# Optimization experiments

Measured on AMD Instinct MI355X. Metric: run time of the kernel, lower is better.

The kernel has to match this reference:

```python
import jax, jax.numpy as jnp
import numpy as np

TOP_K = 2
EPS = 1e-9


def setup_inputs() -> dict:
    key = jax.random.key(0)
    ks = jax.random.split(key, 5)
    B, S, D, H, E, G = 4, 2048, 1024, 1024, 8, 256
    x = jax.random.normal(ks[0], (B, S, D), dtype=jnp.float32)
    # gate MLP (top_k_gating with hidden_size=gating_size)
    Wg1 = jax.random.normal(ks[1], (D, G), dtype=jnp.float32) * (1.0 / np.sqrt(D))
    Wg2 = jax.random.normal(ks[2], (G, E), dtype=jnp.float32) * (1.0 / np.sqrt(G))
    # experts: uniform(-1/D, 1/D) as in init_experts
    W_in = jax.random.uniform(ks[3], (E, D, H), dtype=jnp.float32, minval=-1.0 / D, maxval=1.0 / D)
    W_out = jax.random.uniform(ks[4], (E, H, D), dtype=jnp.float32, minval=-1.0 / D, maxval=1.0 / D)
    return {"x": x, "Wg1": Wg1, "Wg2": Wg2, "W_in": W_in, "W_out": W_out}


def _gate(xf, Wg1, Wg2):
    # gate MLP -> softmax probs over experts
    h = jnp.tanh(xf @ Wg1)                      # [N, G]
    probs = jax.nn.softmax(h @ Wg2, axis=-1)    # [N, E]
    top_v, top_i = jax.lax.top_k(probs, TOP_K)  # [N, k]
    N, E = probs.shape
    # dense gate matrix: zeros except top-k entries (== compute_gating combine weights)
    gates = jnp.zeros((N, E), probs.dtype).at[jnp.arange(N)[:, None], top_i].set(top_v)
    return gates, probs


def _mi_loss(probs):
    # mutual-information aux loss: minimize -(H(mean_p) - mean H(p))
    p_mean = probs.mean(axis=0)
    h_mean = -jnp.sum(p_mean * jnp.log(p_mean + EPS))
    mean_h = -jnp.mean(jnp.sum(probs * jnp.log(probs + EPS), axis=-1))
    return -h_mean + mean_h


def reference(x, Wg1, Wg2, W_in, W_out):
    B, S, D = x.shape
    xf = x.reshape(-1, D)                        # [N, D]
    gates, probs = _gate(xf, Wg1, Wg2)           # [N, E]
    # per-expert FFN: relu(x @ W_in[e]) @ W_out[e], combined with top-k gates.
    h = jnp.einsum('nd,edh->enh', xf, W_in)      # [E, N, H]
    h = jax.nn.relu(h)
    y = jnp.einsum('enh,ehd->end', h, W_out)     # [E, N, D]
    out = jnp.einsum('ne,end->nd', gates, y)     # gate-weighted combine
    loss = _mi_loss(probs)
    return out.reshape(B, S, D), loss
```

## Files before the change

### kernel.cpp

```cpp
#include <hip/hip_runtime.h>


#define N_TOK 8192
#define DIM   1024
#define HID   1024
#define NEXP  8
#define GDIM  256
#define NPAIR (N_TOK * 2)
#define HB_ROWS (NPAIR + 256)
#define MT2   72
#define GAP_P 2e-3f
#define SPLIT_SCALE 2048.0f

typedef __attribute__((ext_vector_type(4))) float    f32x4;
typedef __attribute__((ext_vector_type(8))) _Float16 f16x8;

static __device__ __forceinline__ void async_ld16(const void* g, void* l) {
  __builtin_amdgcn_global_load_lds(
      (const __attribute__((address_space(1))) unsigned int*)g,
      (__attribute__((address_space(3))) unsigned int*)l, 16, 0, 0);
}

__global__ __launch_bounds__(256) void prep1_kernel(const float* __restrict__ Wg1,
                                                    _Float16* __restrict__ WhT,
                                                    _Float16* __restrict__ WlT,
                                                    int* __restrict__ hdr) {
  __shared__ float t[64][65];
  int bx = blockIdx.x;
  int tid = threadIdx.x;
  if (bx < 64) {
    int k0 = (bx & 15) * 64, g0 = (bx >> 4) * 64;
    int col4 = tid & 15, ib = tid >> 4;
#pragma unroll
    for (int q = 0; q < 4; ++q) {
      int i = ib * 4 + q;
      *(float4*)&t[i][col4 * 4] = *(const float4*)&Wg1[(size_t)(k0 + i) * GDIM + g0 + col4 * 4];
    }
    __syncthreads();
#pragma unroll
    for (int q = 0; q < 2; ++q) {
      int c = tid * 2 + q;
      int j = c >> 3, i8 = (c & 7) * 8;
      f16x8 h, l;
#pragma unroll
      for (int k = 0; k < 8; ++k) {
        float v = t[i8 + k][j];
        _Float16 hi = (_Float16)v;
        h[k] = hi;
        l[k] = (_Float16)((v - (float)hi) * SPLIT_SCALE);
      }
      *(f16x8*)&WhT[(size_t)(g0 + j) * DIM + k0 + i8] = h;
      *(f16x8*)&WlT[(size_t)(g0 + j) * DIM + k0 + i8] = l;
    }
  } else {
    hdr[tid * 2 + 0] = 0;
    hdr[tid * 2 + 1] = 0;
  }
}

__global__ __launch_bounds__(256) void gate_cast_kernel(const float* __restrict__ x,
                                                        _Float16* __restrict__ xh,
                                                        const _Float16* __restrict__ WhT,
                                                        const _Float16* __restrict__ WlT,
                                                        const float* __restrict__ Wg2,
                                                        int* __restrict__ top_i,
                                                        float* __restrict__ top_v,
                                                        float* __restrict__ lossacc,
                                                        int* __restrict__ counts,
                                                        int* __restrict__ nflag,
                                                        int* __restrict__ flaglist,
                                                        const float* __restrict__ Win,
                                                        const float* __restrict__ Wout,
                                                        _Float16* __restrict__ WinT,
                                                        _Float16* __restrict__ WoutT) {
  __shared__ __align__(16) char smem[34816];
  int bx = blockIdx.x;
  int tid = threadIdx.x;

  if (bx >= 256) {
    float (*t)[65] = (float(*)[65])smem;
    int b = bx - 256;
    int z = b >> 8, rem = b & 255;
    const float* src = (z < NEXP ? Win : Wout) + (size_t)(z & 7) * DIM * HID;
    _Float16*    dst = (z < NEXP ? WinT : WoutT) + (size_t)(z & 7) * DIM * HID;
    int i0 = (rem & 15) * 64, j0 = (rem >> 4) * 64;
    int col4 = tid & 15, ib = tid >> 4;
#pragma unroll
    for (int q = 0; q < 4; ++q) {
      int i = ib * 4 + q;
      *(float4*)&t[i][col4 * 4] = *(const float4*)&src[(size_t)(i0 + i) * 1024 + j0 + col4 * 4];
    }
    __syncthreads();
#pragma unroll
    for (int q = 0; q < 2; ++q) {
      int c = tid * 2 + q;
      int j = c >> 3, i8 = (c & 7) * 8;
      f16x8 h;
#pragma unroll
      for (int k = 0; k < 8; ++k) h[k] = (_Float16)t[i8 + k][j];
      *(f16x8*)&dst[(size_t)(j0 + j) * 1024 + i0 + i8] = h;
    }
    return;
  }

  _Float16* Ah = (_Float16*)smem;
  _Float16* Bh = (_Float16*)(smem + 2048);
  _Float16* Bl = (_Float16*)(smem + 18432);
  __shared__ float psum[8];
  __shared__ float entsum;
  __shared__ int cnts[8];
  int m0 = bx * 32;
  int lane = tid & 63, wave = tid >> 6;
  int wr = (wave >> 1) * 16;
  int wc = (wave & 1) * 128;
  if (tid < 8) { psum[tid] = 0.f; cnts[tid] = 0; }
  if (tid == 0) entsum = 0.f;

  int arow = tid >> 2, aslt = tid & 3;
  size_t axoff = (size_t)(m0 + arow) * DIM + ((aslt ^ ((arow >> 2) & 3)) << 3);
  _Float16* adst = Ah + tid * 8;
  int srcslot = ((lane & 3) ^ ((lane >> 4) & 3)) << 3;
  size_t bsrc[4];
#pragma unroll
  for (int p = 0; p < 4; ++p)
    bsrc[p] = (size_t)(wave * 16 + p * 64 + (lane >> 2)) * DIM + srcslot;
  int rdoff = ((lane >> 4) ^ ((lane >> 2) & 3)) << 3;
  f32x4 acc[8] = {}, accl[8] = {};

  for (int k0 = 0; k0 < DIM; k0 += 32) {
    __syncthreads();
    if (tid < 128) {
      float4 v0 = *(const float4*)(x + axoff + k0);
      float4 v1 = *(const float4*)(x + axoff + k0 + 4);
      f16x8 hv;
      hv[0] = (_Float16)v0.x; hv[1] = (_Float16)v0.y;
      hv[2] = (_Float16)v0.z; hv[3] = (_Float16)v0.w;
      hv[4] = (_Float16)v1.x; hv[5] = (_Float16)v1.y;
      hv[6] = (_Float16)v1.z; hv[7] = (_Float16)v1.w;
      *(f16x8*)adst = hv;
      *(f16x8*)(xh + axoff + k0) = hv;
    }
#pragma unroll
    for (int p = 0; p < 4; ++p) {
      async_ld16(WhT + bsrc[p] + k0, Bh + wave * 512 + p * 2048);
      async_ld16(WlT + bsrc[p] + k0, Bl + wave * 512 + p * 2048);
    }
    __syncthreads();
    f16x8 a = *(const f16x8*)&Ah[(wr + (lane & 15)) * 32 + rdoff];
#pragma unroll
    for (int n = 0; n < 8; ++n) {
      f16x8 bh = *(const f16x8*)&Bh[(wc + n * 16 + (lane & 15)) * 32 + rdoff];
      f16x8 bl = *(const f16x8*)&Bl[(wc + n * 16 + (lane & 15)) * 32 + rdoff];
      acc[n]  = __builtin_amdgcn_mfma_f32_16x16x32_f16(a, bh, acc[n], 0, 0, 0);
      accl[n] = __builtin_amdgcn_mfma_f32_16x16x32_f16(a, bl, accl[n], 0, 0, 0);
    }
  }
  __syncthreads();
  float (*hsm)[260] = (float(*)[260])smem;
#pragma unroll
  for (int n = 0; n < 8; ++n) {
#pragma unroll
    for (int i = 0; i < 4; ++i) {
      int row = wr + ((lane >> 4) << 2) + i;
      int col = wc + n * 16 + (lane & 15);
      hsm[row][col] = tanhf(acc[n][i] + accl[n][i] * (1.0f / SPLIT_SCALE));
    }
  }
  __syncthreads();

  int tok = tid >> 3, sl = tid & 7;
  float lg[8] = {0, 0, 0, 0, 0, 0, 0, 0};
#pragma unroll
  for (int j = 0; j < 32; ++j) {
    int g = sl + j * 8;
    float hv = hsm[tok][g];
#pragma unroll
    for (int e = 0; e < 8; ++e) lg[e] = fmaf(hv, Wg2[g * 8 + e], lg[e]);
  }
#pragma unroll
  for (int e = 0; e < 8; ++e) {
    lg[e] += __shfl_xor(lg[e], 4);
    lg[e] += __shfl_xor(lg[e], 2);
    lg[e] += __shfl_xor(lg[e], 1);
  }
  if (sl == 0) {
    int token = m0 + tok;
    float mx = lg[0];
#pragma unroll
    for (int e = 1; e < 8; ++e) mx = fmaxf(mx, lg[e]);
    float p[8], s = 0.f;
#pragma unroll
    for (int e = 0; e < 8; ++e) { p[e] = expf(lg[e] - mx); s += p[e]; }
    float inv = 1.f / s, ent = 0.f;
    int i0 = 0, i1 = 0;
    float v0 = -1.f, v1 = -1.f, v2 = -1.f;
#pragma unroll
    for (int e = 0; e < 8; ++e) {
      p[e] *= inv;
      ent += p[e] * logf(p[e] + 1e-9f);
      if (p[e] > v0)      { v2 = v1; v1 = v0; i1 = i0; v0 = p[e]; i0 = e; }
      else if (p[e] > v1) { v2 = v1; v1 = p[e]; i1 = e; }
      else if (p[e] > v2) { v2 = p[e]; }
    }
    top_i[token * 2 + 0] = i0; top_i[token * 2 + 1] = i1;
    top_v[token * 2 + 0] = v0; top_v[token * 2 + 1] = v1;
    if (v1 - v2 < GAP_P) {
      int ix = atomicAdd(nflag, 1);
      if (ix < 8192) flaglist[ix] = token;
    }
#pragma unroll
    for (int e = 0; e < 8; ++e) atomicAdd(&psum[e], p[e]);
    atomicAdd(&entsum, ent);
    atomicAdd(&cnts[i0], 1);
    atomicAdd(&cnts[i1], 1);
  }
  __syncthreads();
  if (tid < 8) { atomicAdd(&lossacc[tid], psum[tid]); atomicAdd(&counts[tid], cnts[tid]); }
  if (tid == 8) atomicAdd(&lossacc[8], entsum);
}

__global__ __launch_bounds__(256) void regate_kernel(const float* __restrict__ x,
                                                     const float* __restrict__ Wg1,
                                                     const float* __restrict__ Wg2,
                                                     const int* __restrict__ nflag,
                                                     const int* __restrict__ flaglist,
                                                     int* __restrict__ top_i,
                                                     float* __restrict__ top_v,
                                                     int* __restrict__ counts) {
  __shared__ float xs[DIM];
  __shared__ float wsum[4][8];
  int tid = threadIdx.x;
  int nf = *nflag; if (nf > 8192) nf = 8192;
  for (int it = blockIdx.x; it < nf; it += gridDim.x) {
    int token = flaglist[it];
    const float* xr = x + (size_t)token * DIM;
    *(float4*)&xs[tid * 4] = *(const float4*)&xr[tid * 4];
    __syncthreads();
    float s0 = 0.f, s1 = 0.f, s2 = 0.f, s3 = 0.f;
    float s4 = 0.f, s5 = 0.f, s6 = 0.f, s7 = 0.f;
    for (int k = 0; k < DIM; k += 8) {
      s0 = fmaf(xs[k + 0], Wg1[(size_t)(k + 0) * GDIM + tid], s0);
      s1 = fmaf(xs[k + 1], Wg1[(size_t)(k + 1) * GDIM + tid], s1);
      s2 = fmaf(xs[k + 2], Wg1[(size_t)(k + 2) * GDIM + tid], s2);
      s3 = fmaf(xs[k + 3], Wg1[(size_t)(k + 3) * GDIM + tid], s3);
      s4 = fmaf(xs[k + 4], Wg1[(size_t)(k + 4) * GDIM + tid], s4);
      s5 = fmaf(xs[k + 5], Wg1[(size_t)(k + 5) * GDIM + tid], s5);
      s6 = fmaf(xs[k + 6], Wg1[(size_t)(k + 6) * GDIM + tid], s6);
      s7 = fmaf(xs[k + 7], Wg1[(size_t)(k + 7) * GDIM + tid], s7);
    }
    float hgv = tanhf(((s0 + s1) + (s2 + s3)) + ((s4 + s5) + (s6 + s7)));
    float lg[8];
#pragma unroll
    for (int e = 0; e < 8; ++e) lg[e] = hgv * Wg2[tid * 8 + e];
#pragma unroll
    for (int e = 0; e < 8; ++e) {
      lg[e] += __shfl_xor(lg[e], 32);
      lg[e] += __shfl_xor(lg[e], 16);
      lg[e] += __shfl_xor(lg[e], 8);
      lg[e] += __shfl_xor(lg[e], 4);
      lg[e] += __shfl_xor(lg[e], 2);
      lg[e] += __shfl_xor(lg[e], 1);
    }
    int wv = tid >> 6;
    if ((tid & 63) == 0) {
#pragma unroll
      for (int e = 0; e < 8; ++e) wsum[wv][e] = lg[e];
    }
    __syncthreads();
    if (tid == 0) {
      float l[8];
#pragma unroll
      for (int e = 0; e < 8; ++e)
        l[e] = (wsum[0][e] + wsum[1][e]) + (wsum[2][e] + wsum[3][e]);
      float mx = l[0];
#pragma unroll
      for (int e = 1; e < 8; ++e) mx = fmaxf(mx, l[e]);
      float p[8], s = 0.f;
#pragma unroll
      for (int e = 0; e < 8; ++e) { p[e] = expf(l[e] - mx); s += p[e]; }
      float inv = 1.f / s;
      int i0 = 0, i1 = 0;
      float v0 = -1.f, v1 = -1.f;
#pragma unroll
      for (int e = 0; e < 8; ++e) {
        p[e] *= inv;
        if (p[e] > v0)      { v1 = v0; i1 = i0; v0 = p[e]; i0 = e; }
        else if (p[e] > v1) { v1 = p[e]; i1 = e; }
      }
      int oi0 = top_i[token * 2 + 0], oi1 = top_i[token * 2 + 1];
      if (oi0 != i0 || oi1 != i1) {
        atomicSub(&counts[oi0], 1); atomicSub(&counts[oi1], 1);
        atomicAdd(&counts[i0], 1);  atomicAdd(&counts[i1], 1);
      }
      top_i[token * 2 + 0] = i0; top_i[token * 2 + 1] = i1;
      top_v[token * 2 + 0] = v0; top_v[token * 2 + 1] = v1;
    }
    __syncthreads();
  }
}

__global__ __launch_bounds__(256) void fill_kernel(const int* __restrict__ top_i,
                                                   const float* __restrict__ top_v,
                                                   const int* __restrict__ counts,
                                                   int* __restrict__ cursors,
                                                   int* __restrict__ ptok,
                                                   float* __restrict__ pgate,
                                                   int* __restrict__ rowof) {
  __shared__ int lcnt[8];
  __shared__ int lbase[8];
  __shared__ int soff[8];
  int tid = threadIdx.x;
  int n = blockIdx.x * 256 + tid;
  if (tid == 0) {
    int a = 0;
#pragma unroll
    for (int e = 0; e < 8; ++e) { soff[e] = a; a += counts[e]; }
  }
  if (tid < 8) lcnt[tid] = 0;
  __syncthreads();
  int e0 = top_i[n * 2 + 0], e1 = top_i[n * 2 + 1];
  int p0 = atomicAdd(&lcnt[e0], 1);
  int p1 = atomicAdd(&lcnt[e1], 1);
  __syncthreads();
  if (tid < 8) lbase[tid] = atomicAdd(&cursors[tid], lcnt[tid]);
  __syncthreads();
  int r0 = soff[e0] + lbase[e0] + p0;
  int r1 = soff[e1] + lbase[e1] + p1;
  ptok[r0] = n;  pgate[r0] = top_v[n * 2 + 0];  rowof[n * 2 + 0] = r0;
  ptok[r1] = n;  pgate[r1] = top_v[n * 2 + 1];  rowof[n * 2 + 1] = r1;
}

#define GEMM_PIPE(STAGE_EXPR)                                                        \
  STAGE_EXPR(0, 0);                                                                  \
  STAGE_EXPR(32, 1);                                                                 \
  asm volatile("s_waitcnt vmcnt(3)" ::: "memory");                                   \
  __builtin_amdgcn_s_barrier();                                                      \
  int cbuf = 0;                                                                      \
  for (int t = 0; t < 32; ++t) {                                                     \
    f16x8 a[4], b[4];                                                                \
    _Pragma("unroll")                                                                \
    for (int m = 0; m < 4; ++m)                                                      \
      a[m] = *(const f16x8*)&Als[cbuf][(wr + m * 16 + (lane & 15)) * 32 + rdoff];    \
    _Pragma("unroll")                                                                \
    for (int n = 0; n < 4; ++n)                                                      \
      b[n] = *(const f16x8*)&Bls[cbuf][(wc + n * 16 + (lane & 15)) * 32 + rdoff];    \
    asm volatile("s_waitcnt lgkmcnt(0)" ::: "memory");                               \
    __builtin_amdgcn_sched_barrier(0);                                               \
    __builtin_amdgcn_s_barrier();                                                    \
    bool st = (t + 2 < 32);                                                          \
    if (st) { STAGE_EXPR((t + 2) * 32, cbuf); }                                      \
    __builtin_amdgcn_s_setprio(1);                                                   \
    _Pragma("unroll")                                                                \
    for (int m = 0; m < 4; ++m)                                                      \
      _Pragma("unroll")                                                              \
      for (int n = 0; n < 4; ++n)                                                    \
        acc[m][n] = __builtin_amdgcn_mfma_f32_16x16x32_f16(a[m], b[n], acc[m][n], 0, 0, 0); \
    __builtin_amdgcn_s_setprio(0);                                                   \
    if (st) asm volatile("s_waitcnt vmcnt(3)" ::: "memory");                         \
    else    asm volatile("s_waitcnt vmcnt(0)" ::: "memory");                         \
    __builtin_amdgcn_sched_barrier(0);                                               \
    __builtin_amdgcn_s_barrier();                                                    \
    cbuf ^= 1;                                                                       \
  }

__global__ __launch_bounds__(512) void gemm1_kernel(const _Float16* __restrict__ xh,
                                                    const _Float16* __restrict__ WinT,
                                                    _Float16* __restrict__ hb,
                                                    const int* __restrict__ counts,
                                                    const int* __restrict__ ptok) {
  __shared__ __align__(16) _Float16 Als[2][256 * 32];
  __shared__ __align__(16) _Float16 Bls[2][128 * 32];
  int bx = blockIdx.x;
  int loc = (bx & 7) * 9 + (bx >> 3);
  int base = 0, cnt = 0, e;
  for (e = 0; e < NEXP; ++e) {
    cnt = counts[e];
    int mts = (cnt + 255) >> 8;
    if (loc < mts) break;
    loc -= mts; base += cnt;
  }
  if (e == NEXP) return;
  int row0 = base + (loc << 8);
  int rmax = cnt - (loc << 8);
  int n0 = blockIdx.y << 7;
  int tid = threadIdx.x, wave = tid >> 6, lane = tid & 63;
  int wr = (wave >> 1) << 6, wc = (wave & 1) << 6;

  const _Float16* WB = WinT + (size_t)e * DIM * HID;
  int scol = (((lane & 3) ^ (lane >> 4)) << 3);
  size_t asrc[2];
#pragma unroll
  for (int j = 0; j < 2; ++j) {
    int r = wave * 32 + j * 16 + (lane >> 2);
    int tok = ptok[(r < rmax) ? (row0 + r) : base];
    asrc[j] = (size_t)tok * DIM + scol;
  }
  int brow = tid >> 2;
  size_t bsrc = (size_t)(n0 + brow) * DIM + (((tid & 3) ^ ((tid >> 4) & 3)) << 3);
  int aldst = wave * 1024;
  int bldst = wave * 512;
  int rdoff = ((lane >> 4) ^ ((lane >> 2) & 3)) << 3;
  f32x4 acc[4][4] = {};

#define STAGE1(K0, CB)                                          \
  do {                                                          \
    async_ld16(xh + asrc[0] + (K0), &Als[(CB)][aldst]);         \
    async_ld16(xh + asrc[1] + (K0), &Als[(CB)][aldst + 512]);   \
    async_ld16(WB + bsrc + (K0), &Bls[(CB)][bldst]);            \
  } while (0)

  GEMM_PIPE(STAGE1)
#undef STAGE1

#pragma unroll
  for (int m = 0; m < 4; ++m) {
#pragma unroll
    for (int i = 0; i < 4; ++i) {
      int r = wr + m * 16 + ((lane >> 4) << 2) + i;
      if (r < rmax) {
        _Float16* hrow = hb + (size_t)(row0 + r) * HID;
#pragma unroll
        for (int n = 0; n < 4; ++n)
          hrow[n0 + wc + n * 16 + (lane & 15)] = (_Float16)fmaxf(acc[m][n][i], 0.f);
      }
    }
  }
}

__global__ __launch_bounds__(512) void gemm2_kernel(const _Float16* __restrict__ hb,
                                                    const _Float16* __restrict__ WoutT,
                                                    _Float16* __restrict__ yb,
                                                    const int* __restrict__ counts,
                                                    const float* __restrict__ pgate) {
  __shared__ __align__(16) _Float16 Als[2][256 * 32];
  __shared__ __align__(16) _Float16 Bls[2][128 * 32];
  int bx = blockIdx.x;
  int loc = (bx & 7) * 9 + (bx >> 3);
  int base = 0, cnt = 0, e;
  for (e = 0; e < NEXP; ++e) {
    cnt = counts[e];
    int mts = (cnt + 255) >> 8;
    if (loc < mts) break;
    loc -= mts; base += cnt;
  }
  if (e == NEXP) return;
  int row0 = base + (loc << 8);
  int rmax = cnt - (loc << 8);
  int n0 = blockIdx.y << 7;
  int tid = threadIdx.x, wave = tid >> 6, lane = tid & 63;
  int wr = (wave >> 1) << 6, wc = (wave & 1) << 6;

  const _Float16* WB = WoutT + (size_t)e * DIM * HID;
  int scol = (((lane & 3) ^ (lane >> 4)) << 3);
  size_t asrc[2];
#pragma unroll
  for (int j = 0; j < 2; ++j) {
    int r = wave * 32 + j * 16 + (lane >> 2);
    asrc[j] = (size_t)(row0 + r) * HID + scol;
  }
  int brow = tid >> 2;
  size_t bsrc = (size_t)(n0 + brow) * DIM + (((tid & 3) ^ ((tid >> 4) & 3)) << 3);
  int aldst = wave * 1024;
  int bldst = wave * 512;
  int rdoff = ((lane >> 4) ^ ((lane >> 2) & 3)) << 3;
  f32x4 acc[4][4] = {};

#define STAGE2(K0, CB)                                          \
  do {                                                          \
    async_ld16(hb + asrc[0] + (K0), &Als[(CB)][aldst]);         \
    async_ld16(hb + asrc[1] + (K0), &Als[(CB)][aldst + 512]);   \
    async_ld16(WB + bsrc + (K0), &Bls[(CB)][bldst]);            \
  } while (0)

  GEMM_PIPE(STAGE2)
#undef STAGE2

#pragma unroll
  for (int m = 0; m < 4; ++m) {
#pragma unroll
    for (int i = 0; i < 4; ++i) {
      int r = wr + m * 16 + ((lane >> 4) << 2) + i;
      if (r < rmax) {
        int gr = row0 + r;
        float gv = pgate[gr];
        _Float16* yrow = yb + (size_t)gr * DIM;
#pragma unroll
        for (int n = 0; n < 4; ++n)
          yrow[n0 + wc + n * 16 + (lane & 15)] = (_Float16)(gv * acc[m][n][i]);
      }
    }
  }
}

__global__ __launch_bounds__(256) void combine_kernel(const _Float16* __restrict__ yb,
                                                      const int* __restrict__ rowof,
                                                      float* __restrict__ out,
                                                      const float* __restrict__ lossacc,
                                                      float* __restrict__ lossdst) {
  int tid = threadIdx.x;
  int token = blockIdx.x * 2 + (tid >> 7);
  int d0 = (tid & 127) * 8;
  int r0 = rowof[token * 2 + 0];
  int r1 = rowof[token * 2 + 1];
  f16x8 a = *(const f16x8*)&yb[(size_t)r0 * DIM + d0];
  f16x8 b = *(const f16x8*)&yb[(size_t)r1 * DIM + d0];
  float* orow = out + (size_t)token * DIM + d0;
  float4 o0, o1;
  o0.x = (float)a[0] + (float)b[0]; o0.y = (float)a[1] + (float)b[1];
  o0.z = (float)a[2] + (float)b[2]; o0.w = (float)a[3] + (float)b[3];
  o1.x = (float)a[4] + (float)b[4]; o1.y = (float)a[5] + (float)b[5];
  o1.z = (float)a[6] + (float)b[6]; o1.w = (float)a[7] + (float)b[7];
  *(float4*)orow = o0;
  *(float4*)(orow + 4) = o1;
  if (blockIdx.x == 0 && tid == 0) {
    float t1 = 0.f;
#pragma unroll
    for (int e = 0; e < 8; ++e) {
      float pm = lossacc[e] * (1.f / (float)N_TOK);
      t1 += pm * logf(pm + 1e-9f);
    }
    lossdst[0] = t1 - lossacc[8] * (1.f / (float)N_TOK);
  }
}

extern "C" void kernel_launch(void* const* d_in, const int* in_sizes, int n_in,
                              void* d_out, int out_size, void* d_ws, size_t ws_size,
                              hipStream_t stream) {
  const float* x    = (const float*)d_in[0];
  const float* Wg1  = (const float*)d_in[1];
  const float* Wg2  = (const float*)d_in[2];
  const float* Win  = (const float*)d_in[3];
  const float* Wout = (const float*)d_in[4];
  float* out = (float*)d_out;

  char* ws = (char*)d_ws;
  size_t off = 0;
  auto alloc = [&](size_t bytes) -> void* {
    void* p = ws + off;
    off = (off + bytes + 255) & ~(size_t)255;
    return p;
  };
  int*   counts  = (int*)alloc(32);
  int*   cursors = (int*)alloc(32);
  float* lossacc = (float*)alloc(64);
  int*   nflag   = (int*)alloc(32);
  int*   flaglist= (int*)alloc(8192 * 4);
  int*   top_i   = (int*)alloc((size_t)NPAIR * 4);
  float* top_v   = (float*)alloc((size_t)NPAIR * 4);
  int*   ptok    = (int*)alloc((size_t)NPAIR * 4);
  float* pgate   = (float*)alloc((size_t)NPAIR * 4);
  int*   rowof   = (int*)alloc((size_t)NPAIR * 4);
  char*  scratch1 = (char*)alloc((size_t)HB_ROWS * HID * 2);
  _Float16* Wg1hT  = (_Float16*)scratch1;
  _Float16* Wg1lsT = Wg1hT + (size_t)GDIM * DIM;
  _Float16* hb     = (_Float16*)scratch1;
  _Float16* xh    = (_Float16*)alloc((size_t)N_TOK * DIM * 2);
  _Float16* WinT  = (_Float16*)alloc((size_t)NEXP * DIM * HID * 2);
  _Float16* WoutT = (_Float16*)alloc((size_t)NEXP * DIM * HID * 2);
  _Float16* yb = xh;
  (void)ws_size; (void)in_sizes; (void)n_in;

  prep1_kernel<<<65, 256, 0, stream>>>(Wg1, Wg1hT, Wg1lsT, (int*)d_ws);
  gate_cast_kernel<<<256 + 4096, 256, 0, stream>>>(x, xh, Wg1hT, Wg1lsT, Wg2,
                                                   top_i, top_v, lossacc, counts,
                                                   nflag, flaglist,
                                                   Win, Wout, WinT, WoutT);
  regate_kernel<<<256, 256, 0, stream>>>(x, Wg1, Wg2, nflag, flaglist, top_i, top_v, counts);
  fill_kernel<<<N_TOK / 256, 256, 0, stream>>>(top_i, top_v, counts, cursors,
                                               ptok, pgate, rowof);
  gemm1_kernel<<<dim3(MT2, HID / 128), 512, 0, stream>>>(xh, WinT, hb, counts, ptok);
  gemm2_kernel<<<dim3(MT2, DIM / 128), 512, 0, stream>>>(hb, WoutT, yb, counts, pgate);
  combine_kernel<<<N_TOK / 2, 256, 0, stream>>>(yb, rowof, out, lossacc,
                                                out + (size_t)N_TOK * DIM);
}
```

Measured before the change: 246.4 us.

## Double-buffer gate GEMM with async prefetch and explicit waitcnt pipelining

```diff
diff --git a/kernel.cpp b/kernel.cpp
--- a/kernel.cpp
+++ b/kernel.cpp
@@ -14,6 +14,7 @@
 
 typedef __attribute__((ext_vector_type(4))) float    f32x4;
 typedef __attribute__((ext_vector_type(8))) _Float16 f16x8;
+typedef __attribute__((ext_vector_type(4))) _Float16 f16x4;
 
 static __device__ __forceinline__ void async_ld16(const void* g, void* l) {
   __builtin_amdgcn_global_load_lds(
@@ -73,7 +74,7 @@
                                                         const float* __restrict__ Wout,
                                                         _Float16* __restrict__ WinT,
                                                         _Float16* __restrict__ WoutT) {
-  __shared__ __align__(16) char smem[34816];
+  __shared__ __align__(16) char smem[69632];
   int bx = blockIdx.x;
   int tid = threadIdx.x;
 
@@ -103,9 +104,6 @@
     return;
   }
 
-  _Float16* Ah = (_Float16*)smem;
-  _Float16* Bh = (_Float16*)(smem + 2048);
-  _Float16* Bl = (_Float16*)(smem + 18432);
   __shared__ float psum[8];
   __shared__ float entsum;
   __shared__ int cnts[8];
@@ -116,46 +114,97 @@
   if (tid < 8) { psum[tid] = 0.f; cnts[tid] = 0; }
   if (tid == 0) entsum = 0.f;
 
-  int arow = tid >> 2, aslt = tid & 3;
-  size_t axoff = (size_t)(m0 + arow) * DIM + ((aslt ^ ((arow >> 2) & 3)) << 3);
-  _Float16* adst = Ah + tid * 8;
+  int arw = tid >> 3, au = tid & 7;
+  size_t axbase = (size_t)(m0 + arw) * DIM +
+                  (((au >> 1) ^ ((arw >> 2) & 3)) * 8 + (au & 1) * 4);
+  int aoff = arw * 32 + au * 4;
   int srcslot = ((lane & 3) ^ ((lane >> 4) & 3)) << 3;
   size_t bsrc[4];
 #pragma unroll
   for (int p = 0; p < 4; ++p)
     bsrc[p] = (size_t)(wave * 16 + p * 64 + (lane >> 2)) * DIM + srcslot;
   int rdoff = ((lane >> 4) ^ ((lane >> 2) & 3)) << 3;
+  size_t xhoff = (size_t)(m0 + wr + (lane & 15)) * DIM + ((lane >> 4) << 3);
   f32x4 acc[8] = {}, accl[8] = {};
-
-  for (int k0 = 0; k0 < DIM; k0 += 32) {
-    __syncthreads();
-    if (tid < 128) {
-      float4 v0 = *(const float4*)(x + axoff + k0);
-      float4 v1 = *(const float4*)(x + axoff + k0 + 4);
-      f16x8 hv;
-      hv[0] = (_Float16)v0.x; hv[1] = (_Float16)v0.y;
-      hv[2] = (_Float16)v0.z; hv[3] = (_Float16)v0.w;
-      hv[4] = (_Float16)v1.x; hv[5] = (_Float16)v1.y;
-      hv[6] = (_Float16)v1.z; hv[7] = (_Float16)v1.w;
-      *(f16x8*)adst = hv;
-      *(f16x8*)(xh + axoff + k0) = hv;
-    }
-#pragma unroll
-    for (int p = 0; p < 4; ++p) {
-      async_ld16(WhT + bsrc[p] + k0, Bh + wave * 512 + p * 2048);
-      async_ld16(WlT + bsrc[p] + k0, Bl + wave * 512 + p * 2048);
-    }
-    __syncthreads();
+  float4 xv;
+
+#define AH(c) ((_Float16*)(smem + (c) * 2048))
+#define BH(c) ((_Float16*)(smem + 4096 + (c) * 16384))
+#define BL(c) ((_Float16*)(smem + 36864 + (c) * 16384))
+#define CVT_W(dstp)                                            \
+  do {                                                         \
+    f16x4 h4;                                                  \
+    h4[0] = (_Float16)xv.x; h4[1] = (_Float16)xv.y;            \
+    h4[2] = (_Float16)xv.z; h4[3] = (_Float16)xv.w;            \
+    *(f16x4*)(dstp) = h4;                                      \
+  } while (0)
+#define ASYNCB(KK, C)                                                        \
+  do {                                                                       \
+    _Pragma("unroll")                                                        \
+    for (int p = 0; p < 4; ++p) {                                            \
+      async_ld16(WhT + bsrc[p] + (KK), BH(C) + wave * 512 + p * 2048);       \
+      async_ld16(WlT + bsrc[p] + (KK), BL(C) + wave * 512 + p * 2048);       \
+    }                                                                        \
+  } while (0)
+
+  xv = *(const float4*)(x + axbase);
+  CVT_W(AH(0) + aoff);
+  xv = *(const float4*)(x + axbase + 32);
+  CVT_W(AH(1) + aoff);
+  __builtin_amdgcn_sched_barrier(0);
+  ASYNCB(0, 0);
+  __builtin_amdgcn_sched_barrier(0);
+  xv = *(const float4*)(x + axbase + 64);
+  __builtin_amdgcn_sched_barrier(0);
+  ASYNCB(32, 1);
+  asm volatile("s_waitcnt vmcnt(9)" ::: "memory");
+  asm volatile("s_waitcnt lgkmcnt(0)" ::: "memory");
+  __builtin_amdgcn_sched_barrier(0);
+  __builtin_amdgcn_s_barrier();
+
+  for (int v = 0; v < 32; ++v) {
+    int cb = v & 1;
+    _Float16* Ah = AH(cb);
+    _Float16* Bh = BH(cb);
+    _Float16* Bl = BL(cb);
     f16x8 a = *(const f16x8*)&Ah[(wr + (lane & 15)) * 32 + rdoff];
+    f16x8 bh[8], bl[8];
 #pragma unroll
     for (int n = 0; n < 8; ++n) {
-      f16x8 bh = *(const f16x8*)&Bh[(wc + n * 16 + (lane & 15)) * 32 + rdoff];
-      f16x8 bl = *(const f16x8*)&Bl[(wc + n * 16 + (lane & 15)) * 32 + rdoff];
-      acc[n]  = __builtin_amdgcn_mfma_f32_16x16x32_f16(a, bh, acc[n], 0, 0, 0);
-      accl[n] = __builtin_amdgcn_mfma_f32_16x16x32_f16(a, bl, accl[n], 0, 0, 0);
-    }
-  }
-  __syncthreads();
+      bh[n] = *(const f16x8*)&Bh[(wc + n * 16 + (lane & 15)) * 32 + rdoff];
+      bl[n] = *(const f16x8*)&Bl[(wc + n * 16 + (lane & 15)) * 32 + rdoff];
+    }
+    *(f16x8*)(xh + xhoff + (size_t)v * 32) = a;
+    asm volatile("s_waitcnt lgkmcnt(0)" ::: "memory");
+    __builtin_amdgcn_sched_barrier(0);
+    __builtin_amdgcn_s_barrier();
+    if (v < 30) {
+      CVT_W(Ah + aoff);
+      __builtin_amdgcn_sched_barrier(0);
+      int kk = (v + 3 < 32 ? v + 3 : 31) * 32;
+      xv = *(const float4*)(x + axbase + kk);
+      __builtin_amdgcn_sched_barrier(0);
+      ASYNCB((v + 2) * 32, cb);
+    }
+    __builtin_amdgcn_s_setprio(1);
+#pragma unroll
+    for (int n = 0; n < 8; ++n) {
+      acc[n]  = __builtin_amdgcn_mfma_f32_16x16x32_f16(a, bh[n], acc[n], 0, 0, 0);
+      accl[n] = __builtin_amdgcn_mfma_f32_16x16x32_f16(a, bl[n], accl[n], 0, 0, 0);
+    }
+    __builtin_amdgcn_s_setprio(0);
+    if (v < 30) asm volatile("s_waitcnt vmcnt(9)" ::: "memory");
+    else        asm volatile("s_waitcnt vmcnt(0)" ::: "memory");
+    asm volatile("s_waitcnt lgkmcnt(0)" ::: "memory");
+    __builtin_amdgcn_sched_barrier(0);
+    __builtin_amdgcn_s_barrier();
+  }
+#undef AH
+#undef BH
+#undef BL
+#undef CVT_W
+#undef ASYNCB
+
   float (*hsm)[260] = (float(*)[260])smem;
 #pragma unroll
   for (int n = 0; n < 8; ++n) {
```

Result: faster. 240.2 us, median of 2 (-2.6%).

## Double-buffer gate GEMM with async prefetch and split hi/lo weight passes

Applied to the files above, without the earlier changes.

```diff
diff --git a/kernel.cpp b/kernel.cpp
--- a/kernel.cpp
+++ b/kernel.cpp
@@ -14,6 +14,7 @@
 
 typedef __attribute__((ext_vector_type(4))) float    f32x4;
 typedef __attribute__((ext_vector_type(8))) _Float16 f16x8;
+typedef __attribute__((ext_vector_type(4))) _Float16 f16x4;
 
 static __device__ __forceinline__ void async_ld16(const void* g, void* l) {
   __builtin_amdgcn_global_load_lds(
@@ -73,7 +74,7 @@
                                                         const float* __restrict__ Wout,
                                                         _Float16* __restrict__ WinT,
                                                         _Float16* __restrict__ WoutT) {
-  __shared__ __align__(16) char smem[34816];
+  __shared__ __align__(16) char smem[36864];
   int bx = blockIdx.x;
   int tid = threadIdx.x;
 
@@ -103,9 +104,6 @@
     return;
   }
 
-  _Float16* Ah = (_Float16*)smem;
-  _Float16* Bh = (_Float16*)(smem + 2048);
-  _Float16* Bl = (_Float16*)(smem + 18432);
   __shared__ float psum[8];
   __shared__ float entsum;
   __shared__ int cnts[8];
@@ -116,46 +114,95 @@
   if (tid < 8) { psum[tid] = 0.f; cnts[tid] = 0; }
   if (tid == 0) entsum = 0.f;
 
-  int arow = tid >> 2, aslt = tid & 3;
-  size_t axoff = (size_t)(m0 + arow) * DIM + ((aslt ^ ((arow >> 2) & 3)) << 3);
-  _Float16* adst = Ah + tid * 8;
+  int arw = tid >> 3, au = tid & 7;
+  size_t axbase = (size_t)(m0 + arw) * DIM +
+                  (((au >> 1) ^ ((arw >> 2) & 3)) * 8 + (au & 1) * 4);
+  int aoff = arw * 32 + au * 4;
   int srcslot = ((lane & 3) ^ ((lane >> 4) & 3)) << 3;
   size_t bsrc[4];
 #pragma unroll
   for (int p = 0; p < 4; ++p)
     bsrc[p] = (size_t)(wave * 16 + p * 64 + (lane >> 2)) * DIM + srcslot;
   int rdoff = ((lane >> 4) ^ ((lane >> 2) & 3)) << 3;
+  size_t xhoff = (size_t)(m0 + wr + (lane & 15)) * DIM + ((lane >> 4) << 3);
   f32x4 acc[8] = {}, accl[8] = {};
-
-  for (int k0 = 0; k0 < DIM; k0 += 32) {
-    __syncthreads();
-    if (tid < 128) {
-      float4 v0 = *(const float4*)(x + axoff + k0);
-      float4 v1 = *(const float4*)(x + axoff + k0 + 4);
-      f16x8 hv;
-      hv[0] = (_Float16)v0.x; hv[1] = (_Float16)v0.y;
-      hv[2] = (_Float16)v0.z; hv[3] = (_Float16)v0.w;
-      hv[4] = (_Float16)v1.x; hv[5] = (_Float16)v1.y;
-      hv[6] = (_Float16)v1.z; hv[7] = (_Float16)v1.w;
-      *(f16x8*)adst = hv;
-      *(f16x8*)(xh + axoff + k0) = hv;
-    }
-#pragma unroll
-    for (int p = 0; p < 4; ++p) {
-      async_ld16(WhT + bsrc[p] + k0, Bh + wave * 512 + p * 2048);
-      async_ld16(WlT + bsrc[p] + k0, Bl + wave * 512 + p * 2048);
-    }
-    __syncthreads();
-    f16x8 a = *(const f16x8*)&Ah[(wr + (lane & 15)) * 32 + rdoff];
-#pragma unroll
-    for (int n = 0; n < 8; ++n) {
-      f16x8 bh = *(const f16x8*)&Bh[(wc + n * 16 + (lane & 15)) * 32 + rdoff];
-      f16x8 bl = *(const f16x8*)&Bl[(wc + n * 16 + (lane & 15)) * 32 + rdoff];
-      acc[n]  = __builtin_amdgcn_mfma_f32_16x16x32_f16(a, bh, acc[n], 0, 0, 0);
-      accl[n] = __builtin_amdgcn_mfma_f32_16x16x32_f16(a, bl, accl[n], 0, 0, 0);
-    }
-  }
-  __syncthreads();
+  float4 xv;
+
+#define AH(c) ((_Float16*)(smem + (c) * 2048))
+#define B2(c) ((_Float16*)(smem + 4096 + (c) * 16384))
+#define CVT_W(dstp)                                            \
+  do {                                                         \
+    f16x4 h4;                                                  \
+    h4[0] = (_Float16)xv.x; h4[1] = (_Float16)xv.y;            \
+    h4[2] = (_Float16)xv.z; h4[3] = (_Float16)xv.w;            \
+    *(f16x4*)(dstp) = h4;                                      \
+  } while (0)
+#define ASYNCB4(KK, C, WSRC)                                                 \
+  do {                                                                       \
+    _Pragma("unroll")                                                        \
+    for (int p = 0; p < 4; ++p)                                              \
+      async_ld16(WSRC + bsrc[p] + (KK), B2(C) + wave * 512 + p * 2048);      \
+  } while (0)
+
+#define GATE_PASS(WSRC, ACCARR, EMIT)                                        \
+  do {                                                                       \
+    xv = *(const float4*)(x + axbase);                                       \
+    CVT_W(AH(0) + aoff);                                                     \
+    xv = *(const float4*)(x + axbase + 32);                                  \
+    CVT_W(AH(1) + aoff);                                                     \
+    __builtin_amdgcn_sched_barrier(0);                                       \
+    ASYNCB4(0, 0, WSRC);                                                     \
+    __builtin_amdgcn_sched_barrier(0);                                       \
+    xv = *(const float4*)(x + axbase + 64);                                  \
+    __builtin_amdgcn_sched_barrier(0);                                       \
+    ASYNCB4(32, 1, WSRC);                                                    \
+    asm volatile("s_waitcnt vmcnt(5)" ::: "memory");                         \
+    asm volatile("s_waitcnt lgkmcnt(0)" ::: "memory");                       \
+    __builtin_amdgcn_sched_barrier(0);                                       \
+    __builtin_amdgcn_s_barrier();                                            \
+    for (int v = 0; v < 32; ++v) {                                           \
+      int cb = v & 1;                                                        \
+      _Float16* Ah = AH(cb);                                                 \
+      _Float16* Bb = B2(cb);                                                 \
+      f16x8 a = *(const f16x8*)&Ah[(wr + (lane & 15)) * 32 + rdoff];         \
+      f16x8 bfr[8];                                                          \
+      _Pragma("unroll")                                                      \
+      for (int n = 0; n < 8; ++n)                                            \
+        bfr[n] = *(const f16x8*)&Bb[(wc + n * 16 + (lane & 15)) * 32 + rdoff]; \
+      if (EMIT) *(f16x8*)(xh + xhoff + (size_t)v * 32) = a;                  \
+      asm volatile("s_waitcnt lgkmcnt(0)" ::: "memory");                     \
+      __builtin_amdgcn_sched_barrier(0);                                     \
+      __builtin_amdgcn_s_barrier();                                          \
+      if (v < 30) {                                                          \
+        CVT_W(Ah + aoff);                                                    \
+        __builtin_amdgcn_sched_barrier(0);                                   \
+        int kk = (v + 3 < 32 ? v + 3 : 31) * 32;                             \
+        xv = *(const float4*)(x + axbase + kk);                              \
+        __builtin_amdgcn_sched_barrier(0);                                   \
+        ASYNCB4((v + 2) * 32, cb, WSRC);                                     \
+      }                                                                      \
+      __builtin_amdgcn_s_setprio(1);                                         \
+      _Pragma("unroll")                                                      \
+      for (int n = 0; n < 8; ++n)                                            \
+        ACCARR[n] = __builtin_amdgcn_mfma_f32_16x16x32_f16(a, bfr[n], ACCARR[n], 0, 0, 0); \
+      __builtin_amdgcn_s_setprio(0);                                         \
+      if (v < 30) asm volatile("s_waitcnt vmcnt(5)" ::: "memory");           \
+      else        asm volatile("s_waitcnt vmcnt(0)" ::: "memory");           \
+      asm volatile("s_waitcnt lgkmcnt(0)" ::: "memory");                     \
+      __builtin_amdgcn_sched_barrier(0);                                     \
+      __builtin_amdgcn_s_barrier();                                          \
+    }                                                                        \
+  } while (0)
+
+  GATE_PASS(WhT, acc, 1);
+  GATE_PASS(WlT, accl, 0);
+
+#undef AH
+#undef B2
+#undef CVT_W
+#undef ASYNCB4
+#undef GATE_PASS
+
   float (*hsm)[260] = (float(*)[260])smem;
 #pragma unroll
   for (int n = 0; n < 8; ++n) {
```

After: 250.9 us. Within noise of the previous version (+1.8%).
